# Performance work log

Measured on AMD Instinct MI355X. Metric: run time of the kernel, lower is better.

## Reference

```python
import jax, jax.numpy as jnp
from jax import lax
import numpy as np

N_CENTER, N_NEAR, COUT = 1024, 32, 256


def fps(xyz, m):
    # farthest point sampling -> [B, m] int32 indices
    B, N, _ = xyz.shape
    dist0 = jnp.full((B, N), 1e10, xyz.dtype)
    far0 = jnp.zeros((B,), jnp.int32)

    def step(carry, _):
        dists, far = carry
        cen = jax.vmap(lambda p, i: p[i])(xyz, far)            # [B,3]
        d = jnp.sum((xyz - cen[:, None, :]) ** 2, axis=-1)     # [B,N]
        dists = jnp.minimum(dists, d)
        nxt = jnp.argmax(dists, axis=-1).astype(jnp.int32)
        return (dists, nxt), far

    _, idx = lax.scan(step, (dist0, far0), None, length=m)
    return jnp.transpose(idx)                                   # [B,m]


def knn(xyz, k):
    # euclidean kNN over all points -> [B,N,k] (stand-in for surface_knn)
    sq = jnp.sum(xyz ** 2, axis=-1)                             # [B,N]
    d = sq[:, :, None] + sq[:, None, :] - 2.0 * jnp.einsum('bnd,bmd->bnm', xyz, xyz)
    _, idx = lax.top_k(-d, k)
    return idx


def gather(x, idx):
    # index_points: x [B,N,...], idx [B,S] or [B,S,K]
    return jax.vmap(lambda p, i: p[i])(x, idx)


def point_attention(center_fea, group_fea, wq, wk, wv):
    # center_fea [B,S,Cin], group_fea [B,S,K,D] -> [B,S,COUT]
    q = jnp.einsum('bsc,ch->bsh', center_fea, wq)
    k = jnp.einsum('bskd,dh->bskh', group_fea, wk)
    v = jnp.einsum('bskd,dh->bskh', group_fea, wv)
    scores = jnp.einsum('bsh,bskh->bsk', q, k) / jnp.sqrt(jnp.asarray(COUT, q.dtype))
    attn = jax.nn.softmax(scores, axis=-1)
    return jnp.einsum('bsk,bskh->bsh', attn, v)


def _forward(xyz, mad, adj, pt, mad_fea, adj_fea, pt_fea, cst_fea,
             wq_mad, wk_mad, wv_mad, wq_adj, wk_adj, wv_adj,
             wq_pt, wk_pt, wv_pt, wq_cst, wk_cst, wv_cst):
    idx_all = knn(xyz, N_NEAR)                  # [B,N,K]
    fps_idx = fps(xyz, N_CENTER)                # [B,S]

    center_xyz = gather(xyz, fps_idx)
    center_mad = gather(mad, fps_idx)
    center_adj = gather(adj, fps_idx)
    center_pt = gather(pt, fps_idx)
    c_mad_fea = gather(mad_fea, fps_idx)
    c_adj_fea = gather(adj_fea, fps_idx)
    c_pt_fea = gather(pt_fea, fps_idx)
    c_cst_fea = gather(cst_fea, fps_idx)

    idx = gather(idx_all, fps_idx)              # [B,S,K]
    g_xyz = gather(xyz, idx)
    g_mad = gather(mad, idx)
    g_adj = gather(adj, idx)
    g_pt = gather(pt, idx)
    g_mad_fea = gather(mad_fea, idx)
    g_adj_fea = gather(adj_fea, idx)
    g_pt_fea = gather(pt_fea, idx)
    g_cst_fea = gather(cst_fea, idx)

    mad_rel = g_mad - center_mad[:, :, None, :]
    adj_cat = jnp.concatenate([g_adj, jnp.broadcast_to(center_adj[:, :, None, :], g_adj.shape)], axis=-1)
    pt_cat = jnp.concatenate([g_pt, jnp.broadcast_to(center_pt[:, :, None, :], g_pt.shape)], axis=-1)
    xyz_rel = g_xyz - center_xyz[:, :, None, :]

    g_mad_fea = jnp.concatenate([g_mad_fea, mad_rel], axis=-1)
    g_adj_fea = jnp.concatenate([g_adj_fea, adj_cat], axis=-1)
    g_pt_fea = jnp.concatenate([g_pt_fea, pt_cat], axis=-1)
    g_cst_fea = jnp.concatenate([g_cst_fea, xyz_rel], axis=-1)

    o_mad = point_attention(c_mad_fea, g_mad_fea, wq_mad, wk_mad, wv_mad)
    o_adj = point_attention(c_adj_fea, g_adj_fea, wq_adj, wk_adj, wv_adj)
    o_pt = point_attention(c_pt_fea, g_pt_fea, wq_pt, wk_pt, wv_pt)
    o_cst = point_attention(c_cst_fea, g_cst_fea, wq_cst, wk_cst, wv_cst)

    return (center_xyz, center_mad, center_adj, center_pt, o_mad, o_adj, o_pt, o_cst)


def setup_inputs() -> dict:
    key = jax.random.key(0)
    ks = jax.random.split(key, 24)
    B, N, C = 4, 4096, 128
    inp = {
        'xyz': jax.random.normal(ks[0], (B, N, 3), jnp.float32),
        'mad': jax.random.normal(ks[1], (B, N, 3), jnp.float32),
        'adj': jax.random.uniform(ks[2], (B, N, 2), jnp.float32),
        'pt': jax.random.uniform(ks[3], (B, N, 4), jnp.float32),
        'mad_fea': jax.random.normal(ks[4], (B, N, C), jnp.float32),
        'adj_fea': jax.random.normal(ks[5], (B, N, C), jnp.float32),
        'pt_fea': jax.random.normal(ks[6], (B, N, C), jnp.float32),
        'cst_fea': jax.random.normal(ks[7], (B, N, C), jnp.float32),
    }
    dims = {'wq_mad': C, 'wk_mad': C + 3, 'wv_mad': C + 3,
            'wq_adj': C, 'wk_adj': C + 4, 'wv_adj': C + 4,
            'wq_pt': C, 'wk_pt': C + 8, 'wv_pt': C + 8,
            'wq_cst': C, 'wk_cst': C + 3, 'wv_cst': C + 3}
    for i, (name, d) in enumerate(dims.items()):
        inp[name] = jax.random.normal(ks[8 + i], (d, COUT), jnp.float32) * 0.02
    return inp


def reference(xyz, mad, adj, pt, mad_fea, adj_fea, pt_fea, cst_fea,
              wq_mad, wk_mad, wv_mad, wq_adj, wk_adj, wv_adj,
              wq_pt, wk_pt, wv_pt, wq_cst, wk_cst, wv_cst):
    return _forward(xyz, mad, adj, pt, mad_fea, adj_fea, pt_fea, cst_fea,
                    wq_mad, wk_mad, wv_mad, wq_adj, wk_adj, wv_adj,
                    wq_pt, wk_pt, wv_pt, wq_cst, wk_cst, wv_cst)
```

## Files before the change

### kernel.cpp

```cpp
#include <hip/hip_runtime.h>

#define BATCH 4
#define NPTS  4096
#define NC    1024
#define KNN   32
#define CIN   128
#define CO    256
#define DP    136

#define OFF_CXYZ 0
#define OFF_CMAD (BATCH*NC*3)
#define OFF_CADJ (OFF_CMAD + BATCH*NC*3)
#define OFF_CPT  (OFF_CADJ + BATCH*NC*2)
#define OFF_OMAD (OFF_CPT  + BATCH*NC*4)
#define OFF_OADJ (OFF_OMAD + BATCH*NC*CO)
#define OFF_OPT  (OFF_OADJ + BATCH*NC*CO)
#define OFF_OCST (OFF_OPT  + BATCH*NC*CO)

typedef unsigned long long u64;

template<bool MAXI>
__device__ __forceinline__ u64 wave_red_u64(u64 k)
{
    const int oldv = MAXI ? 0 : -1;
#define DPP_STEP(C)                                                              \
    {                                                                            \
        unsigned plo = (unsigned)__builtin_amdgcn_update_dpp(oldv, (int)(unsigned)k,        C, 0xf, 0xf, false); \
        unsigned phi = (unsigned)__builtin_amdgcn_update_dpp(oldv, (int)(unsigned)(k>>32),  C, 0xf, 0xf, false); \
        u64 p = ((u64)phi << 32) | plo;                                          \
        if (MAXI ? (p > k) : (p < k)) k = p;                                     \
    }
    DPP_STEP(0x111) DPP_STEP(0x112) DPP_STEP(0x114)
    DPP_STEP(0x118) DPP_STEP(0x142) DPP_STEP(0x143)
#undef DPP_STEP
    return k;
}

__global__ __launch_bounds__(256) void fps_prep_kernel(
    const float* __restrict__ xyz, int* __restrict__ fps_idx,
    const float* __restrict__ wq_mad, const float* __restrict__ wk_mad, const float* __restrict__ wv_mad,
    const float* __restrict__ wq_adj, const float* __restrict__ wk_adj, const float* __restrict__ wv_adj,
    const float* __restrict__ wq_pt,  const float* __restrict__ wk_pt,  const float* __restrict__ wv_pt,
    const float* __restrict__ wq_cst, const float* __restrict__ wk_cst, const float* __restrict__ wv_cst,
    float* __restrict__ M, float* __restrict__ Wvp)
{
    __shared__ float4 s_xyz[NPTS];
    __shared__ u64    s_ck[2][4];
    const int t = threadIdx.x;

    if (blockIdx.x >= BATCH) {
        const int r    = blockIdx.x - BATCH;
        const int type = r / DP;
        const int row  = r - type * DP;
        const float* wq; const float* wk; const float* wv; int D;
        if (type == 0)      { wq=wq_mad; wk=wk_mad; wv=wv_mad; D=131; }
        else if (type == 1) { wq=wq_adj; wk=wk_adj; wv=wv_adj; D=132; }
        else if (type == 2) { wq=wq_pt;  wk=wk_pt;  wv=wv_pt;  D=136; }
        else                { wq=wq_cst; wk=wk_cst; wv=wv_cst; D=131; }

        Wvp[((size_t)type*DP + row)*CO + t] = (row < D) ? wv[(size_t)row*CO + t] : 0.f;

        if (row < CIN) {
            float* sq = (float*)s_xyz;
            sq[t] = wq[(size_t)row*CO + t];
            __syncthreads();
            if (t < DP) {
                float acc = 0.f;
                if (t < D) {
                    const float* wkr = wk + (size_t)t * CO;
                    for (int h = 0; h < CO; h += 4) {
                        float4 a = *(const float4*)&wkr[h];
                        float4 b4 = *(const float4*)&sq[h];
                        acc = fmaf(a.x,b4.x,acc); acc = fmaf(a.y,b4.y,acc);
                        acc = fmaf(a.z,b4.z,acc); acc = fmaf(a.w,b4.w,acc);
                    }
                }
                M[((size_t)type*CIN + row)*DP + t] = acc;
            }
        }
        return;
    }

    const int b = blockIdx.x;
    const float* xb = xyz + (size_t)b * NPTS * 3;

    float px[16], py[16], pz[16], dd[16];
    unsigned inv[16];
#pragma unroll
    for (int i = 0; i < 16; ++i) {
        int p = t + i * 256;
        px[i] = xb[p*3+0]; py[i] = xb[p*3+1]; pz[i] = xb[p*3+2];
        s_xyz[p] = make_float4(px[i], py[i], pz[i], 0.f);
        dd[i] = 1e10f;
        inv[i] = ~(unsigned)p;
    }
    __syncthreads();

    int far = 0;
    float cx = xb[0], cy = xb[1], cz = xb[2];
    for (int s = 0; s < NC; ++s) {
        if (t == 0) fps_idx[b*NC + s] = far;
        u64 K[16];
#pragma unroll
        for (int i = 0; i < 16; ++i) {
            float dx = __fsub_rn(px[i], cx);
            float dy = __fsub_rn(py[i], cy);
            float dz = __fsub_rn(pz[i], cz);
            float d  = __fadd_rn(__fadd_rn(__fmul_rn(dx,dx), __fmul_rn(dy,dy)), __fmul_rn(dz,dz));
            float nd = fminf(dd[i], d);
            dd[i] = nd;
            K[i] = ((u64)__float_as_uint(nd) << 32) | inv[i];
        }
#pragma unroll
        for (int st = 8; st >= 1; st >>= 1)
#pragma unroll
            for (int j = 0; j < st; ++j)
                if (K[j+st] > K[j]) K[j] = K[j+st];
        u64 k = wave_red_u64<true>(K[0]);

        const int buf = s & 1;
        if ((t & 63) == 63) s_ck[buf][t>>6] = k;
        __syncthreads();
        u64 k0 = s_ck[buf][0], k1 = s_ck[buf][1], k2 = s_ck[buf][2], k3 = s_ck[buf][3];
        if (k1 > k0) k0 = k1;
        if (k3 > k2) k2 = k3;
        if (k2 > k0) k0 = k2;
        far = (int)~((unsigned)k0);
        float4 c = s_xyz[far];
        cx = c.x; cy = c.y; cz = c.z;
    }
}

__global__ __launch_bounds__(256) void knn_kernel(const float* __restrict__ xyz,
                                                  const int* __restrict__ fps_idx,
                                                  int* __restrict__ nbr_idx)
{
    const int bs = blockIdx.x;
    const int b  = bs >> 10;
    const int t  = threadIdx.x;
    const float* xb = xyz + (size_t)b * NPTS * 3;
    const int ci = fps_idx[bs];
    const float cx = xb[ci*3], cy = xb[ci*3+1], cz = xb[ci*3+2];
    const float sqc = __fadd_rn(__fadd_rn(__fmul_rn(cx,cx), __fmul_rn(cy,cy)), __fmul_rn(cz,cz));

    u64 key[16];
#pragma unroll
    for (int i = 0; i < 16; ++i) {
        int p = t + i * 256;
        float x = xb[p*3], y = xb[p*3+1], z = xb[p*3+2];
        float sqm = __fadd_rn(__fadd_rn(__fmul_rn(x,x), __fmul_rn(y,y)), __fmul_rn(z,z));
        float dot = __fadd_rn(__fadd_rn(__fmul_rn(cx,x), __fmul_rn(cy,y)), __fmul_rn(cz,z));
        float dv  = __fsub_rn(__fadd_rn(sqc, sqm), __fmul_rn(2.0f, dot));
        unsigned u = __float_as_uint(dv);
        u ^= (unsigned)(((int)u >> 31)) | 0x80000000u;
        key[i] = ((u64)u << 32) | (unsigned)p;
    }
    u64 kmin = key[0];
#pragma unroll
    for (int i = 1; i < 16; ++i) if (key[i] < kmin) kmin = key[i];

    __shared__ u64 s_ck[2][4];

    for (int kk = 0; kk < KNN; ++kk) {
        u64 k = wave_red_u64<false>(kmin);
        const int buf = kk & 1;
        if ((t & 63) == 63) s_ck[buf][t>>6] = k;
        __syncthreads();
        u64 k0 = s_ck[buf][0], k1 = s_ck[buf][1], k2 = s_ck[buf][2], k3 = s_ck[buf][3];
        if (k1 < k0) k0 = k1;
        if (k3 < k2) k2 = k3;
        if (k2 < k0) k0 = k2;
        unsigned w = (unsigned)k0;
        if (t == 0) nbr_idx[bs*KNN + kk] = (int)w;
        if ((w & 255u) == (unsigned)t) {
#pragma unroll
            for (int i = 0; i < 16; ++i)
                if (w == (unsigned)(t + i*256)) key[i] = ~0ull;
            u64 m = key[0];
#pragma unroll
            for (int i = 1; i < 16; ++i) if (key[i] < m) m = key[i];
            kmin = m;
        }
    }
}

template<int TYPE>
__device__ __forceinline__ void attn_t(
    int b, int bs0, int ci,
    const float* __restrict__ fea, const float* __restrict__ aux,
    const float* __restrict__ Mt, const float* __restrict__ Wvpt,
    float* __restrict__ outp,
    float (*s_cf)[CIN], float (*s_u)[DP], float (*s_fea)[KNN][DP],
    float (*s_sc)[KNN], float (*s_wf)[DP], const int (*s_nbr4)[KNN])
{
    const int t = threadIdx.x, g = t >> 6, l = t & 63;
    const int l31 = l & 31, h32 = l >> 5;

    if (l < 32) {
        float4 v = *(const float4*)&fea[((size_t)(b*NPTS + ci))*CIN + l*4];
        *(float4*)&s_cf[g][l*4] = v;
    }
#pragma unroll
    for (int it = 0; it < 16; ++it) {
        int kk = it*2 + h32;
        int j  = s_nbr4[g][kk];
        float4 v = *(const float4*)&fea[((size_t)(b*NPTS + j))*CIN + l31*4];
        *(float4*)&s_fea[g][kk][l31*4] = v;
    }
    if (l < KNN) {
        int j = s_nbr4[g][l];
        float pad[8];
        if (TYPE == 0 || TYPE == 3) {
#pragma unroll
            for (int i = 0; i < 3; ++i)
                pad[i] = aux[(size_t)(b*NPTS + j)*3 + i] - aux[(size_t)(b*NPTS + ci)*3 + i];
            pad[3]=pad[4]=pad[5]=pad[6]=pad[7]=0.f;
        } else if (TYPE == 1) {
            pad[0] = aux[(size_t)(b*NPTS + j)*2 + 0];
            pad[1] = aux[(size_t)(b*NPTS + j)*2 + 1];
            pad[2] = aux[(size_t)(b*NPTS + ci)*2 + 0];
            pad[3] = aux[(size_t)(b*NPTS + ci)*2 + 1];
            pad[4]=pad[5]=pad[6]=pad[7]=0.f;
        } else {
#pragma unroll
            for (int i = 0; i < 4; ++i) pad[i]   = aux[(size_t)(b*NPTS + j)*4 + i];
#pragma unroll
            for (int i = 0; i < 4; ++i) pad[4+i] = aux[(size_t)(b*NPTS + ci)*4 + i];
        }
#pragma unroll
        for (int i = 0; i < 8; ++i) s_fea[g][l][CIN+i] = pad[i];
    }
    __syncthreads();

#pragma unroll
    for (int j = 0; j < 3; ++j) {
        int d = l + 64*j;
        if (d < DP) {
            float acc = 0.f;
            for (int c = 0; c < CIN; c += 4) {
                float4 cf4 = *(const float4*)&s_cf[g][c];
                acc = fmaf(cf4.x, Mt[(size_t)(c+0)*DP + d], acc);
                acc = fmaf(cf4.y, Mt[(size_t)(c+1)*DP + d], acc);
                acc = fmaf(cf4.z, Mt[(size_t)(c+2)*DP + d], acc);
                acc = fmaf(cf4.w, Mt[(size_t)(c+3)*DP + d], acc);
            }
            s_u[g][d] = acc;
        }
    }
    __syncthreads();

#pragma unroll
    for (int it = 0; it < 16; ++it) {
        int kk = it*2 + h32;
        float acc = 0.f;
        for (int c = l31; c < DP/4; c += 32) {
            float4 f4 = *(const float4*)&s_fea[g][kk][c*4];
            float4 u4 = *(const float4*)&s_u[g][c*4];
            acc = fmaf(f4.x,u4.x,acc); acc = fmaf(f4.y,u4.y,acc);
            acc = fmaf(f4.z,u4.z,acc); acc = fmaf(f4.w,u4.w,acc);
        }
#pragma unroll
        for (int off = 16; off; off >>= 1) acc += __shfl_xor(acc, off);
        if (l31 == 0) s_sc[g][kk] = acc * 0.0625f;
    }
    __syncthreads();

    if (l < KNN) {
        float sc = s_sc[g][l];
        float m = sc;
#pragma unroll
        for (int off = 16; off; off >>= 1) m = fmaxf(m, __shfl_xor(m, off));
        float e = expf(sc - m);
        float ssum = e;
#pragma unroll
        for (int off = 16; off; off >>= 1) ssum += __shfl_xor(ssum, off);
        s_sc[g][l] = e / ssum;
    }
    __syncthreads();

    if (l < DP/4) {
        const int d0 = l*4;
        float w0=0.f, w1=0.f, w2=0.f, w3=0.f;
#pragma unroll
        for (int k4 = 0; k4 < KNN; k4 += 4) {
            float4 a  = *(const float4*)&s_sc[g][k4];
            float4 f0 = *(const float4*)&s_fea[g][k4+0][d0];
            float4 f1 = *(const float4*)&s_fea[g][k4+1][d0];
            float4 f2 = *(const float4*)&s_fea[g][k4+2][d0];
            float4 f3 = *(const float4*)&s_fea[g][k4+3][d0];
            w0=fmaf(a.x,f0.x,w0); w1=fmaf(a.x,f0.y,w1); w2=fmaf(a.x,f0.z,w2); w3=fmaf(a.x,f0.w,w3);
            w0=fmaf(a.y,f1.x,w0); w1=fmaf(a.y,f1.y,w1); w2=fmaf(a.y,f1.z,w2); w3=fmaf(a.y,f1.w,w3);
            w0=fmaf(a.z,f2.x,w0); w1=fmaf(a.z,f2.y,w1); w2=fmaf(a.z,f2.z,w2); w3=fmaf(a.z,f2.w,w3);
            w0=fmaf(a.w,f3.x,w0); w1=fmaf(a.w,f3.y,w1); w2=fmaf(a.w,f3.z,w2); w3=fmaf(a.w,f3.w,w3);
        }
        s_wf[g][d0+0]=w0; s_wf[g][d0+1]=w1; s_wf[g][d0+2]=w2; s_wf[g][d0+3]=w3;
    }
    __syncthreads();

    float o0=0.f, o1=0.f, o2=0.f, o3=0.f;
    for (int d4 = 0; d4 < DP/4; ++d4) {
        float4 wf0 = *(const float4*)&s_wf[0][d4*4];
        float4 wf1 = *(const float4*)&s_wf[1][d4*4];
        float4 wf2 = *(const float4*)&s_wf[2][d4*4];
        float4 wf3 = *(const float4*)&s_wf[3][d4*4];
        float v0 = Wvpt[(size_t)(d4*4+0)*CO + t];
        float v1 = Wvpt[(size_t)(d4*4+1)*CO + t];
        float v2 = Wvpt[(size_t)(d4*4+2)*CO + t];
        float v3 = Wvpt[(size_t)(d4*4+3)*CO + t];
        o0=fmaf(wf0.x,v0,o0); o0=fmaf(wf0.y,v1,o0); o0=fmaf(wf0.z,v2,o0); o0=fmaf(wf0.w,v3,o0);
        o1=fmaf(wf1.x,v0,o1); o1=fmaf(wf1.y,v1,o1); o1=fmaf(wf1.z,v2,o1); o1=fmaf(wf1.w,v3,o1);
        o2=fmaf(wf2.x,v0,o2); o2=fmaf(wf2.y,v1,o2); o2=fmaf(wf2.z,v2,o2); o2=fmaf(wf2.w,v3,o2);
        o3=fmaf(wf3.x,v0,o3); o3=fmaf(wf3.y,v1,o3); o3=fmaf(wf3.z,v2,o3); o3=fmaf(wf3.w,v3,o3);
    }
    outp[(size_t)(bs0+0)*CO + t] = o0;
    outp[(size_t)(bs0+1)*CO + t] = o1;
    outp[(size_t)(bs0+2)*CO + t] = o2;
    outp[(size_t)(bs0+3)*CO + t] = o3;
    __syncthreads();
}

__global__ __launch_bounds__(256) void attn_kernel(
    const float* __restrict__ xyz, const float* __restrict__ mad,
    const float* __restrict__ adj, const float* __restrict__ pt,
    const float* __restrict__ mad_fea, const float* __restrict__ adj_fea,
    const float* __restrict__ pt_fea,  const float* __restrict__ cst_fea,
    const float* __restrict__ M, const float* __restrict__ Wvp,
    const int* __restrict__ fps_idx, const int* __restrict__ nbr_idx,
    float* __restrict__ out)
{
    __shared__ float s_cf[4][CIN];
    __shared__ float s_u[4][DP];
    __shared__ float s_fea[4][KNN][DP];
    __shared__ float s_sc[4][KNN];
    __shared__ float s_wf[4][DP];
    __shared__ int   s_nbr4[4][KNN];
    __shared__ int   s_ci4[4];

    const int bs0 = blockIdx.x * 4;
    const int b   = bs0 >> 10;
    const int t   = threadIdx.x;
    const int g   = t >> 6, l = t & 63;

    if (t < 4) s_ci4[t] = fps_idx[bs0 + t];
    if (t < 128) s_nbr4[t>>5][t&31] = nbr_idx[(bs0 + (t>>5))*KNN + (t&31)];
    __syncthreads();
    const int ci = s_ci4[g];

    if (l < 3)             out[OFF_CXYZ + (bs0+g)*3 + l]      = xyz[(size_t)(b*NPTS+ci)*3 + l];
    if (l >= 4 && l < 7)   out[OFF_CMAD + (bs0+g)*3 + (l-4)]  = mad[(size_t)(b*NPTS+ci)*3 + (l-4)];
    if (l >= 8 && l < 10)  out[OFF_CADJ + (bs0+g)*2 + (l-8)]  = adj[(size_t)(b*NPTS+ci)*2 + (l-8)];
    if (l >= 12 && l < 16) out[OFF_CPT  + (bs0+g)*4 + (l-12)] = pt[(size_t)(b*NPTS+ci)*4 + (l-12)];

    attn_t<0>(b, bs0, ci, mad_fea, mad, M + 0*CIN*DP, Wvp + 0*DP*CO, out + OFF_OMAD,
              s_cf, s_u, s_fea, s_sc, s_wf, s_nbr4);
    attn_t<1>(b, bs0, ci, adj_fea, adj, M + 1*CIN*DP, Wvp + 1*DP*CO, out + OFF_OADJ,
              s_cf, s_u, s_fea, s_sc, s_wf, s_nbr4);
    attn_t<2>(b, bs0, ci, pt_fea,  pt,  M + 2*CIN*DP, Wvp + 2*DP*CO, out + OFF_OPT,
              s_cf, s_u, s_fea, s_sc, s_wf, s_nbr4);
    attn_t<3>(b, bs0, ci, cst_fea, xyz, M + 3*CIN*DP, Wvp + 3*DP*CO, out + OFF_OCST,
              s_cf, s_u, s_fea, s_sc, s_wf, s_nbr4);
}

extern "C" void kernel_launch(void* const* d_in, const int* in_sizes, int n_in,
                              void* d_out, int out_size, void* d_ws, size_t ws_size,
                              hipStream_t stream)
{
    const float* xyz     = (const float*)d_in[0];
    const float* mad     = (const float*)d_in[1];
    const float* adj     = (const float*)d_in[2];
    const float* pt      = (const float*)d_in[3];
    const float* mad_fea = (const float*)d_in[4];
    const float* adj_fea = (const float*)d_in[5];
    const float* pt_fea  = (const float*)d_in[6];
    const float* cst_fea = (const float*)d_in[7];
    const float* wq_mad  = (const float*)d_in[8];
    const float* wk_mad  = (const float*)d_in[9];
    const float* wv_mad  = (const float*)d_in[10];
    const float* wq_adj  = (const float*)d_in[11];
    const float* wk_adj  = (const float*)d_in[12];
    const float* wv_adj  = (const float*)d_in[13];
    const float* wq_pt   = (const float*)d_in[14];
    const float* wk_pt   = (const float*)d_in[15];
    const float* wv_pt   = (const float*)d_in[16];
    const float* wq_cst  = (const float*)d_in[17];
    const float* wk_cst  = (const float*)d_in[18];
    const float* wv_cst  = (const float*)d_in[19];
    float* out = (float*)d_out;

    int*   fps_idx = (int*)d_ws;
    int*   nbr_idx = fps_idx + BATCH*NC;
    float* M       = (float*)(nbr_idx + BATCH*NC*KNN);
    float* Wvp     = M + 4*CIN*DP;

    fps_prep_kernel<<<BATCH + 4*DP, 256, 0, stream>>>(xyz, fps_idx,
        wq_mad, wk_mad, wv_mad, wq_adj, wk_adj, wv_adj,
        wq_pt, wk_pt, wv_pt, wq_cst, wk_cst, wv_cst, M, Wvp);
    knn_kernel<<<BATCH*NC, 256, 0, stream>>>(xyz, fps_idx, nbr_idx);
    attn_kernel<<<BATCH*NC/4, 256, 0, stream>>>(xyz, mad, adj, pt,
        mad_fea, adj_fea, pt_fea, cst_fea, M, Wvp, fps_idx, nbr_idx, out);
}
```

Before: 1.120 ms.

## Fuse kNN selection into attention kernel and widen FPS block to 512 threads

Drops the separate kNN kernel. Each wavefront in the attention kernel now computes its own center's 32 nearest neighbours: it keeps 64 distances in registers with grouped minima and runs 32 wave-level DPP argmin rounds with no block barrier. The FPS block grows to 512 threads with 8 points per thread, which shortens the serial per-step reduction chain but adds a second level of cross-wave combining. The changes also remove the nbr_idx global round trip and one launch, and set a two-block occupancy hint on the attention kernel. The cost is heavier register pressure from the 64-entry distance array, which may cause spills or lower occupancy.

New measurement: 1.176 ms. 1.05x slower.

```diff
diff --git a/kernel.cpp b/kernel.cpp
--- a/kernel.cpp
+++ b/kernel.cpp
@@ -36,7 +36,7 @@
     return k;
 }
 
-__global__ __launch_bounds__(256) void fps_prep_kernel(
+__global__ __launch_bounds__(512) void fps_prep_kernel(
     const float* __restrict__ xyz, int* __restrict__ fps_idx,
     const float* __restrict__ wq_mad, const float* __restrict__ wk_mad, const float* __restrict__ wv_mad,
     const float* __restrict__ wq_adj, const float* __restrict__ wk_adj, const float* __restrict__ wv_adj,
@@ -45,7 +45,7 @@
     float* __restrict__ M, float* __restrict__ Wvp)
 {
     __shared__ float4 s_xyz[NPTS];
-    __shared__ u64    s_ck[2][4];
+    __shared__ u64    s_ck[2][8];
     const int t = threadIdx.x;
 
     if (blockIdx.x >= BATCH) {
@@ -58,11 +58,12 @@
         else if (type == 2) { wq=wq_pt;  wk=wk_pt;  wv=wv_pt;  D=136; }
         else                { wq=wq_cst; wk=wk_cst; wv=wv_cst; D=131; }
 
-        Wvp[((size_t)type*DP + row)*CO + t] = (row < D) ? wv[(size_t)row*CO + t] : 0.f;
+        if (t < CO)
+            Wvp[((size_t)type*DP + row)*CO + t] = (row < D) ? wv[(size_t)row*CO + t] : 0.f;
 
         if (row < CIN) {
             float* sq = (float*)s_xyz;
-            sq[t] = wq[(size_t)row*CO + t];
+            if (t < CO) sq[t] = wq[(size_t)row*CO + t];
             __syncthreads();
             if (t < DP) {
                 float acc = 0.f;
@@ -84,11 +85,11 @@
     const int b = blockIdx.x;
     const float* xb = xyz + (size_t)b * NPTS * 3;
 
-    float px[16], py[16], pz[16], dd[16];
-    unsigned inv[16];
-#pragma unroll
-    for (int i = 0; i < 16; ++i) {
-        int p = t + i * 256;
+    float px[8], py[8], pz[8], dd[8];
+    unsigned inv[8];
+#pragma unroll
+    for (int i = 0; i < 8; ++i) {
+        int p = t + i * 512;
         px[i] = xb[p*3+0]; py[i] = xb[p*3+1]; pz[i] = xb[p*3+2];
         s_xyz[p] = make_float4(px[i], py[i], pz[i], 0.f);
         dd[i] = 1e10f;
@@ -100,9 +101,9 @@
     float cx = xb[0], cy = xb[1], cz = xb[2];
     for (int s = 0; s < NC; ++s) {
         if (t == 0) fps_idx[b*NC + s] = far;
-        u64 K[16];
-#pragma unroll
-        for (int i = 0; i < 16; ++i) {
+        u64 K[8];
+#pragma unroll
+        for (int i = 0; i < 8; ++i) {
             float dx = __fsub_rn(px[i], cx);
             float dy = __fsub_rn(py[i], cy);
             float dz = __fsub_rn(pz[i], cz);
@@ -112,7 +113,7 @@
             K[i] = ((u64)__float_as_uint(nd) << 32) | inv[i];
         }
 #pragma unroll
-        for (int st = 8; st >= 1; st >>= 1)
+        for (int st = 4; st >= 1; st >>= 1)
 #pragma unroll
             for (int j = 0; j < st; ++j)
                 if (K[j+st] > K[j]) K[j] = K[j+st];
@@ -121,66 +122,15 @@
         const int buf = s & 1;
         if ((t & 63) == 63) s_ck[buf][t>>6] = k;
         __syncthreads();
-        u64 k0 = s_ck[buf][0], k1 = s_ck[buf][1], k2 = s_ck[buf][2], k3 = s_ck[buf][3];
-        if (k1 > k0) k0 = k1;
-        if (k3 > k2) k2 = k3;
-        if (k2 > k0) k0 = k2;
-        far = (int)~((unsigned)k0);
+        u64 c0 = s_ck[buf][0], c1 = s_ck[buf][1], c2 = s_ck[buf][2], c3 = s_ck[buf][3];
+        u64 c4 = s_ck[buf][4], c5 = s_ck[buf][5], c6 = s_ck[buf][6], c7 = s_ck[buf][7];
+        if (c1 > c0) c0 = c1;  if (c3 > c2) c2 = c3;
+        if (c5 > c4) c4 = c5;  if (c7 > c6) c6 = c7;
+        if (c2 > c0) c0 = c2;  if (c6 > c4) c4 = c6;
+        if (c4 > c0) c0 = c4;
+        far = (int)~((unsigned)c0);
         float4 c = s_xyz[far];
         cx = c.x; cy = c.y; cz = c.z;
-    }
-}
-
-__global__ __launch_bounds__(256) void knn_kernel(const float* __restrict__ xyz,
-                                                  const int* __restrict__ fps_idx,
-                                                  int* __restrict__ nbr_idx)
-{
-    const int bs = blockIdx.x;
-    const int b  = bs >> 10;
-    const int t  = threadIdx.x;
-    const float* xb = xyz + (size_t)b * NPTS * 3;
-    const int ci = fps_idx[bs];
-    const float cx = xb[ci*3], cy = xb[ci*3+1], cz = xb[ci*3+2];
-    const float sqc = __fadd_rn(__fadd_rn(__fmul_rn(cx,cx), __fmul_rn(cy,cy)), __fmul_rn(cz,cz));
-
-    u64 key[16];
-#pragma unroll
-    for (int i = 0; i < 16; ++i) {
-        int p = t + i * 256;
-        float x = xb[p*3], y = xb[p*3+1], z = xb[p*3+2];
-        float sqm = __fadd_rn(__fadd_rn(__fmul_rn(x,x), __fmul_rn(y,y)), __fmul_rn(z,z));
-        float dot = __fadd_rn(__fadd_rn(__fmul_rn(cx,x), __fmul_rn(cy,y)), __fmul_rn(cz,z));
-        float dv  = __fsub_rn(__fadd_rn(sqc, sqm), __fmul_rn(2.0f, dot));
-        unsigned u = __float_as_uint(dv);
-        u ^= (unsigned)(((int)u >> 31)) | 0x80000000u;
-        key[i] = ((u64)u << 32) | (unsigned)p;
-    }
-    u64 kmin = key[0];
-#pragma unroll
-    for (int i = 1; i < 16; ++i) if (key[i] < kmin) kmin = key[i];
-
-    __shared__ u64 s_ck[2][4];
-
-    for (int kk = 0; kk < KNN; ++kk) {
-        u64 k = wave_red_u64<false>(kmin);
-        const int buf = kk & 1;
-        if ((t & 63) == 63) s_ck[buf][t>>6] = k;
-        __syncthreads();
-        u64 k0 = s_ck[buf][0], k1 = s_ck[buf][1], k2 = s_ck[buf][2], k3 = s_ck[buf][3];
-        if (k1 < k0) k0 = k1;
-        if (k3 < k2) k2 = k3;
-        if (k2 < k0) k0 = k2;
-        unsigned w = (unsigned)k0;
-        if (t == 0) nbr_idx[bs*KNN + kk] = (int)w;
-        if ((w & 255u) == (unsigned)t) {
-#pragma unroll
-            for (int i = 0; i < 16; ++i)
-                if (w == (unsigned)(t + i*256)) key[i] = ~0ull;
-            u64 m = key[0];
-#pragma unroll
-            for (int i = 1; i < 16; ++i) if (key[i] < m) m = key[i];
-            kmin = m;
-        }
     }
 }
 
@@ -319,13 +269,13 @@
     __syncthreads();
 }
 
-__global__ __launch_bounds__(256) void attn_kernel(
+__global__ __launch_bounds__(256, 2) void attn_kernel(
     const float* __restrict__ xyz, const float* __restrict__ mad,
     const float* __restrict__ adj, const float* __restrict__ pt,
     const float* __restrict__ mad_fea, const float* __restrict__ adj_fea,
     const float* __restrict__ pt_fea,  const float* __restrict__ cst_fea,
     const float* __restrict__ M, const float* __restrict__ Wvp,
-    const int* __restrict__ fps_idx, const int* __restrict__ nbr_idx,
+    const int* __restrict__ fps_idx,
     float* __restrict__ out)
 {
     __shared__ float s_cf[4][CIN];
@@ -334,22 +284,79 @@
     __shared__ float s_sc[4][KNN];
     __shared__ float s_wf[4][DP];
     __shared__ int   s_nbr4[4][KNN];
-    __shared__ int   s_ci4[4];
 
     const int bs0 = blockIdx.x * 4;
     const int b   = bs0 >> 10;
     const int t   = threadIdx.x;
     const int g   = t >> 6, l = t & 63;
-
-    if (t < 4) s_ci4[t] = fps_idx[bs0 + t];
-    if (t < 128) s_nbr4[t>>5][t&31] = nbr_idx[(bs0 + (t>>5))*KNN + (t&31)];
-    __syncthreads();
-    const int ci = s_ci4[g];
-
-    if (l < 3)             out[OFF_CXYZ + (bs0+g)*3 + l]      = xyz[(size_t)(b*NPTS+ci)*3 + l];
+    const float* xb = xyz + (size_t)b * NPTS * 3;
+
+    const int ci = fps_idx[bs0 + g];
+
+    if (l < 3)             out[OFF_CXYZ + (bs0+g)*3 + l]      = xb[(size_t)ci*3 + l];
     if (l >= 4 && l < 7)   out[OFF_CMAD + (bs0+g)*3 + (l-4)]  = mad[(size_t)(b*NPTS+ci)*3 + (l-4)];
     if (l >= 8 && l < 10)  out[OFF_CADJ + (bs0+g)*2 + (l-8)]  = adj[(size_t)(b*NPTS+ci)*2 + (l-8)];
     if (l >= 12 && l < 16) out[OFF_CPT  + (bs0+g)*4 + (l-12)] = pt[(size_t)(b*NPTS+ci)*4 + (l-12)];
+
+    {
+        const float cx = xb[ci*3], cy = xb[ci*3+1], cz = xb[ci*3+2];
+        const float sqc = __fadd_rn(__fadd_rn(__fmul_rn(cx,cx), __fmul_rn(cy,cy)), __fmul_rn(cz,cz));
+
+        unsigned du[64];
+#pragma unroll
+        for (int j = 0; j < 64; ++j) {
+            int p = l + (j << 6);
+            float x = xb[p*3], y = xb[p*3+1], z = xb[p*3+2];
+            float sqm = __fadd_rn(__fadd_rn(__fmul_rn(x,x), __fmul_rn(y,y)), __fmul_rn(z,z));
+            float dot = __fadd_rn(__fadd_rn(__fmul_rn(cx,x), __fmul_rn(cy,y)), __fmul_rn(cz,z));
+            float dv  = __fsub_rn(__fadd_rn(sqc, sqm), __fmul_rn(2.0f, dot));
+            unsigned u = __float_as_uint(dv);
+            u ^= (unsigned)(((int)u >> 31)) | 0x80000000u;
+            du[j] = u;
+        }
+        u64 gk[4];
+#pragma unroll
+        for (int G2 = 0; G2 < 4; ++G2) {
+            int j0 = G2*16;
+            u64 m = ((u64)du[j0] << 32) | (unsigned)(l + (j0 << 6));
+#pragma unroll
+            for (int jj = 1; jj < 16; ++jj) {
+                int j = j0 + jj;
+                u64 kj = ((u64)du[j] << 32) | (unsigned)(l + (j << 6));
+                if (kj < m) m = kj;
+            }
+            gk[G2] = m;
+        }
+
+        for (int kk = 0; kk < KNN; ++kk) {
+            u64 m01 = gk[0] < gk[1] ? gk[0] : gk[1];
+            u64 m23 = gk[2] < gk[3] ? gk[2] : gk[3];
+            u64 kmin = m01 < m23 ? m01 : m23;
+            u64 kw = wave_red_u64<false>(kmin);
+            int widx = __shfl((int)(unsigned)kw, 63);
+            if (l == 0) s_nbr4[g][kk] = widx;
+            int wj = widx >> 6;
+            if ((widx & 63) == l) {
+#pragma unroll
+                for (int G2 = 0; G2 < 4; ++G2) {
+                    if ((wj >> 4) == G2) {
+#pragma unroll
+                        for (int jj = 0; jj < 16; ++jj)
+                            if (wj == G2*16 + jj) du[G2*16 + jj] = 0xFFFFFFFFu;
+                        int j0 = G2*16;
+                        u64 m = ((u64)du[j0] << 32) | (unsigned)(l + (j0 << 6));
+#pragma unroll
+                        for (int jj = 1; jj < 16; ++jj) {
+                            int j = j0 + jj;
+                            u64 kj = ((u64)du[j] << 32) | (unsigned)(l + (j << 6));
+                            if (kj < m) m = kj;
+                        }
+                        gk[G2] = m;
+                    }
+                }
+            }
+        }
+    }
 
     attn_t<0>(b, bs0, ci, mad_fea, mad, M + 0*CIN*DP, Wvp + 0*DP*CO, out + OFF_OMAD,
               s_cf, s_u, s_fea, s_sc, s_wf, s_nbr4);
@@ -388,14 +395,12 @@
     float* out = (float*)d_out;
 
     int*   fps_idx = (int*)d_ws;
-    int*   nbr_idx = fps_idx + BATCH*NC;
-    float* M       = (float*)(nbr_idx + BATCH*NC*KNN);
+    float* M       = (float*)(fps_idx + BATCH*NC);
     float* Wvp     = M + 4*CIN*DP;
 
-    fps_prep_kernel<<<BATCH + 4*DP, 256, 0, stream>>>(xyz, fps_idx,
+    fps_prep_kernel<<<BATCH + 4*DP, 512, 0, stream>>>(xyz, fps_idx,
         wq_mad, wk_mad, wv_mad, wq_adj, wk_adj, wv_adj,
         wq_pt, wk_pt, wv_pt, wq_cst, wk_cst, wv_cst, M, Wvp);
-    knn_kernel<<<BATCH*NC, 256, 0, stream>>>(xyz, fps_idx, nbr_idx);
     attn_kernel<<<BATCH*NC/4, 256, 0, stream>>>(xyz, mad, adj, pt,
-        mad_fea, adj_fea, pt_fea, cst_fea, M, Wvp, fps_idx, nbr_idx, out);
+        mad_fea, adj_fea, pt_fea, cst_fea, M, Wvp, fps_idx, out);
 }
```
